# Kernel optimization log

Hardware: AMD Instinct MI355X
Metric: run time of the kernel (lower is better)

## Reference

```python
import jax, jax.numpy as jnp
import numpy as np

B, S, D, H, DFF = 4, 2048, 1024, 8, 4096
DH = D // H  # 128
EPS = 1e-5


def layernorm(x, gamma, beta):
    mu = jnp.mean(x, axis=-1, keepdims=True)
    var = jnp.mean(jnp.square(x - mu), axis=-1, keepdims=True)
    return (x - mu) * jax.lax.rsqrt(var + EPS) * gamma + beta


def setup_inputs() -> dict:
    key = jax.random.key(0)
    ks = jax.random.split(key, 6)
    s = 0.02
    return {
        "src": jax.random.normal(ks[0], (B, S, D), jnp.float32),
        "w_qkv": jax.random.normal(ks[1], (D, 3 * D), jnp.float32) * s,
        "w_out": jax.random.normal(ks[2], (D, D), jnp.float32) * s,
        "w1": jax.random.normal(ks[3], (D, DFF), jnp.float32) * s,
        "b1": jnp.zeros((DFF,), jnp.float32),
        "w2": jax.random.normal(ks[4], (DFF, D), jnp.float32) * s,
        "b2": jnp.zeros((D,), jnp.float32),
        "g1": jnp.ones((D,), jnp.float32),
        "beta1": jnp.zeros((D,), jnp.float32),
        "g2": jnp.ones((D,), jnp.float32),
        "beta2": jnp.zeros((D,), jnp.float32),
    }


def reference(src, w_qkv, w_out, w1, b1, w2, b2, g1, beta1, g2, beta2):
    b, s, d = src.shape
    # --- RingAttention == exact causal MHA on a single device ---
    qkv = src @ w_qkv  # [b, s, 3d]
    q, k, v = jnp.split(qkv, 3, axis=-1)
    to_heads = lambda x: x.reshape(b, s, H, DH).transpose(0, 2, 1, 3)  # [b,h,s,dh]
    q, k, v = to_heads(q), to_heads(k), to_heads(v)
    scale = 1.0 / jnp.sqrt(jnp.asarray(DH, src.dtype))
    scores = jnp.einsum('bhqd,bhkd->bhqk', q, k) * scale  # [b,h,s,s]
    causal = jnp.tril(jnp.ones((s, s), bool))
    neg = jnp.asarray(jnp.finfo(src.dtype).min, src.dtype)
    scores = jnp.where(causal, scores, neg)
    attn = jax.nn.softmax(scores, axis=-1)
    o = jnp.einsum('bhqk,bhkd->bhqd', attn, v)  # [b,h,s,dh]
    o = o.transpose(0, 2, 1, 3).reshape(b, s, d) @ w_out
    # dropout layers are identity at inference
    x = layernorm(src + o, g1, beta1)
    ff = jax.nn.relu(x @ w1 + b1) @ w2 + b2
    return layernorm(x + ff, g2, beta2)
```

## Files before the change

### kernel.cpp

```cpp
#include <hip/hip_runtime.h>

typedef unsigned short u16;
typedef __attribute__((ext_vector_type(8))) short short8;
typedef __attribute__((ext_vector_type(4))) float float4v;

#define MFMA_BF16(a, b, c) __builtin_amdgcn_mfma_f32_16x16x32_bf16((a), (b), (c), 0, 0, 0)

#define B_ 4
#define S_ 2048
#define D_ 1024
#define H_ 8
#define DH_ 128
#define DFF_ 4096
#define EPS_ 1e-5f
#define ROWS_ (B_ * S_)
#define CSCALE_ 0.12751672939502f

__device__ __forceinline__ u16 f2bf(float f) {
  union { float f; unsigned u; } x; x.f = f;
  unsigned r = x.u + 0x7fffu + ((x.u >> 16) & 1u);
  return (u16)(r >> 16);
}

typedef __attribute__((address_space(1))) const unsigned int guint;
typedef __attribute__((address_space(3))) unsigned int luint;
__device__ __forceinline__ void gl2lds16(const u16* g, u16* l) {
  __builtin_amdgcn_global_load_lds((guint*)g, (luint*)l, 16, 0, 0);
}

__global__ void cast_bf16_kernel(const float* __restrict__ in, u16* __restrict__ out, int n4) {
  int i = blockIdx.x * blockDim.x + threadIdx.x;
  int stride = gridDim.x * blockDim.x;
  for (; i < n4; i += stride) {
    float4 v = ((const float4*)in)[i];
    ushort4 u;
    u.x = f2bf(v.x); u.y = f2bf(v.y); u.z = f2bf(v.z); u.w = f2bf(v.w);
    ((ushort4*)out)[i] = u;
  }
}

__global__ void transpose_cast_kernel(const float* __restrict__ in, u16* __restrict__ out,
                                      int K, int N) {
  __shared__ float t[32][33];
  int k0 = blockIdx.x * 32, n0 = blockIdx.y * 32;
  int tx = threadIdx.x & 31, ty = threadIdx.x >> 5;
  #pragma unroll
  for (int i = 0; i < 4; ++i)
    t[ty + 8 * i][tx] = in[(size_t)(k0 + ty + 8 * i) * N + n0 + tx];
  __syncthreads();
  #pragma unroll
  for (int i = 0; i < 4; ++i)
    out[(size_t)(n0 + ty + 8 * i) * K + k0 + tx] = f2bf(t[tx][ty + 8 * i]);
}

__global__ void transpose_v_kernel(const u16* __restrict__ in, u16* __restrict__ out) {
  __shared__ u16 t[32][33];
  int s0 = blockIdx.x * 32, d0 = blockIdx.y * 32, bh = blockIdx.z;
  const u16* src = in + (size_t)bh * S_ * DH_;
  u16* dst = out + (size_t)bh * DH_ * S_;
  int tx = threadIdx.x & 31, ty = threadIdx.x >> 5;
  #pragma unroll
  for (int i = 0; i < 4; ++i)
    t[ty + 8 * i][tx] = src[(size_t)(s0 + ty + 8 * i) * DH_ + d0 + tx];
  __syncthreads();
  #pragma unroll
  for (int i = 0; i < 4; ++i)
    dst[(size_t)(d0 + ty + 8 * i) * S_ + s0 + tx] = t[tx][ty + 8 * i];
}

template <int MODE>
__global__ __launch_bounds__(256) void gemm_kernel(
    const u16* __restrict__ A, const u16* __restrict__ Bt,
    const int M, const int N, const int K,
    float* __restrict__ outF, u16* __restrict__ outH, const float* __restrict__ bias,
    u16* __restrict__ qo, u16* __restrict__ ko, u16* __restrict__ vo) {
  __shared__ u16 As[128][32];
  __shared__ u16 Bs[128][32];
  const int tid = threadIdx.x;
  const int lane = tid & 63, wave = tid >> 6;
  const int quad = lane >> 4, r16 = lane & 15;
  const int wm = (wave >> 1) * 64, wn = (wave & 1) * 64;
  const int m0 = blockIdx.x * 128, n0 = blockIdx.y * 128;

  float4v acc[4][4];
  #pragma unroll
  for (int i = 0; i < 4; ++i)
    #pragma unroll
    for (int j = 0; j < 4; ++j) acc[i][j] = (float4v)0.0f;

  const int srow = lane >> 2, sseg = lane & 3;
  const u16* Ag0 = A + (size_t)(m0 + wave * 32 + srow) * K + sseg * 8;
  const u16* Ag1 = Ag0 + (size_t)16 * K;
  const u16* Bg0 = Bt + (size_t)(n0 + wave * 32 + srow) * K + sseg * 8;
  const u16* Bg1 = Bg0 + (size_t)16 * K;
  u16* Al0 = &As[wave * 32][0];
  u16* Al1 = &As[wave * 32 + 16][0];
  u16* Bl0 = &Bs[wave * 32][0];
  u16* Bl1 = &Bs[wave * 32 + 16][0];

  for (int k0 = 0; k0 < K; k0 += 32) {
    __syncthreads();
    gl2lds16(Ag0 + k0, Al0);
    gl2lds16(Ag1 + k0, Al1);
    gl2lds16(Bg0 + k0, Bl0);
    gl2lds16(Bg1 + k0, Bl1);
    __syncthreads();
    short8 af[4], bf[4];
    #pragma unroll
    for (int t = 0; t < 4; ++t) af[t] = *(const short8*)&As[wm + t * 16 + r16][quad * 8];
    #pragma unroll
    for (int t = 0; t < 4; ++t) bf[t] = *(const short8*)&Bs[wn + t * 16 + r16][quad * 8];
    #pragma unroll
    for (int i = 0; i < 4; ++i)
      #pragma unroll
      for (int j = 0; j < 4; ++j) acc[i][j] = MFMA_BF16(af[i], bf[j], acc[i][j]);
  }

  #pragma unroll
  for (int i = 0; i < 4; ++i) {
    const int rowb = m0 + wm + i * 16 + quad * 4;
    #pragma unroll
    for (int j = 0; j < 4; ++j) {
      const int col = n0 + wn + j * 16 + r16;
      #pragma unroll
      for (int rg = 0; rg < 4; ++rg) {
        float val = acc[i][j][rg];
        const int r = rowb + rg;
        if (MODE == 0) {
          const int part = col >> 10, cc = col & 1023;
          const int h = cc >> 7, dh = cc & 127;
          const int b = r >> 11, s = r & 2047;
          u16* dst = (part == 0) ? qo : (part == 1) ? ko : vo;
          if (part == 0) val *= CSCALE_;
          dst[((size_t)(b * H_ + h) * S_ + s) * DH_ + dh] = f2bf(val);
        } else if (MODE == 1) {
          outF[(size_t)r * N + col] = val;
        } else if (MODE == 2) {
          val += bias[col];
          val = fmaxf(val, 0.0f);
          outH[(size_t)r * N + col] = f2bf(val);
        } else {
          val += bias[col];
          outF[(size_t)r * N + col] = val;
        }
      }
    }
  }
}

__global__ __launch_bounds__(256) void attn_kernel(
    const u16* __restrict__ Q, const u16* __restrict__ Kg,
    const u16* __restrict__ Vtg, u16* __restrict__ O) {
  __shared__ u16 Ks[64][136];
  __shared__ u16 Vt[128][72];
  __shared__ u16 Pw[4][16][72];
  const int tid = threadIdx.x;
  const int lane = tid & 63, wave = tid >> 6;
  const int quad = lane >> 4, r16 = lane & 15;
  const int pairIdx = blockIdx.x;
  const int bh = blockIdx.y;
  const size_t base = (size_t)bh * S_ * DH_;
  const size_t vtb = (size_t)bh * DH_ * S_;
  const int b = bh >> 3, h = bh & 7;

  const u16* kg0 = Kg + base + (size_t)(tid >> 4) * DH_ + (tid & 15) * 8;
  u16* ksl = &Ks[tid >> 4][(tid & 15) * 8];
  const u16* vg0 = Vtg + vtb + (size_t)(tid >> 3) * S_ + (tid & 7) * 8;
  u16* vtl = &Vt[tid >> 3][(tid & 7) * 8];

  for (int half = 0; half < 2; ++half) {
    const int qb = (half == 0) ? pairIdx : 31 - pairIdx;
    const int qr = qb * 64 + wave * 16 + r16;

    short8 aq[4];
    #pragma unroll
    for (int ks = 0; ks < 4; ++ks)
      aq[ks] = *(const short8*)(Q + base + (size_t)qr * DH_ + ks * 32 + quad * 8);

    float4v acco[8];
    #pragma unroll
    for (int i = 0; i < 8; ++i) acco[i] = (float4v)0.0f;
    float m_q = -1e30f, l_q = 0.0f;

    for (int kb = 0; kb <= qb; ++kb) {
      __syncthreads();
      #pragma unroll
      for (int i = 0; i < 4; ++i)
        *(short8*)(ksl + i * 16 * 136) =
            *(const short8*)(kg0 + (size_t)(kb * 64 + i * 16) * DH_);
      #pragma unroll
      for (int i = 0; i < 4; ++i)
        *(short8*)(vtl + i * 32 * 72) =
            *(const short8*)(vg0 + (size_t)i * 32 * S_ + kb * 64);
      __syncthreads();

      float4v accs[4];
      #pragma unroll
      for (int t = 0; t < 4; ++t) accs[t] = (float4v)0.0f;
      #pragma unroll
      for (int ks = 0; ks < 4; ++ks) {
        #pragma unroll
        for (int t = 0; t < 4; ++t) {
          short8 ak = *(const short8*)&Ks[t * 16 + r16][ks * 32 + quad * 8];
          accs[t] = MFMA_BF16(ak, aq[ks], accs[t]);
        }
      }
      if (kb == qb) {
        #pragma unroll
        for (int t = 0; t < 4; ++t)
          #pragma unroll
          for (int rg = 0; rg < 4; ++rg) {
            int kc = kb * 64 + t * 16 + quad * 4 + rg;
            if (kc > qr) accs[t][rg] = -1e30f;
          }
      }
      float mv = accs[0][0];
      #pragma unroll
      for (int t = 0; t < 4; ++t)
        #pragma unroll
        for (int rg = 0; rg < 4; ++rg) mv = fmaxf(mv, accs[t][rg]);
      mv = fmaxf(mv, __shfl_xor(mv, 16));
      mv = fmaxf(mv, __shfl_xor(mv, 32));
      const float mnew = fmaxf(m_q, mv);
      const float alpha = __builtin_amdgcn_exp2f(m_q - mnew);
      float s0 = 0.0f;
      #pragma unroll
      for (int t = 0; t < 4; ++t)
        #pragma unroll
        for (int rg = 0; rg < 4; ++rg) {
          float p = __builtin_amdgcn_exp2f(accs[t][rg] - mnew);
          accs[t][rg] = p;
          s0 += p;
        }
      s0 += __shfl_xor(s0, 16);
      s0 += __shfl_xor(s0, 32);
      l_q = l_q * alpha + s0;
      m_q = mnew;

      #pragma unroll
      for (int t = 0; t < 4; ++t) {
        union { float f; unsigned u; } c0, c1, c2, c3;
        c0.f = accs[t][0]; c1.f = accs[t][1]; c2.f = accs[t][2]; c3.f = accs[t][3];
        uint2 pk;
        pk.x = ((c0.u + 0x8000u) >> 16) | ((c1.u + 0x8000u) & 0xffff0000u);
        pk.y = ((c2.u + 0x8000u) >> 16) | ((c3.u + 0x8000u) & 0xffff0000u);
        *(uint2*)&Pw[wave][r16][t * 16 + quad * 4] = pk;
      }
      float al[4];
      #pragma unroll
      for (int rg = 0; rg < 4; ++rg) al[rg] = __shfl(alpha, quad * 4 + rg);
      #pragma unroll
      for (int nt = 0; nt < 8; ++nt)
        #pragma unroll
        for (int rg = 0; rg < 4; ++rg) acco[nt][rg] *= al[rg];
      asm volatile("s_waitcnt lgkmcnt(0)" ::: "memory");
      #pragma unroll
      for (int ks2 = 0; ks2 < 2; ++ks2) {
        short8 ap = *(const short8*)&Pw[wave][r16][ks2 * 32 + quad * 8];
        #pragma unroll
        for (int nt = 0; nt < 8; ++nt) {
          short8 bv = *(const short8*)&Vt[nt * 16 + r16][ks2 * 32 + quad * 8];
          acco[nt] = MFMA_BF16(ap, bv, acco[nt]);
        }
      }
    }

    float lr[4];
    #pragma unroll
    for (int rg = 0; rg < 4; ++rg) lr[rg] = __shfl(l_q, quad * 4 + rg);
    const int sbase = qb * 64 + wave * 16 + quad * 4;
    #pragma unroll
    for (int nt = 0; nt < 8; ++nt)
      #pragma unroll
      for (int rg = 0; rg < 4; ++rg) {
        float val = acco[nt][rg] / lr[rg];
        O[((size_t)(b * S_ + sbase + rg)) * D_ + h * DH_ + nt * 16 + r16] = f2bf(val);
      }
  }
}

__global__ __launch_bounds__(256) void ln_kernel(
    const float* __restrict__ a, const float* __restrict__ res,
    const float* __restrict__ g, const float* __restrict__ be,
    float* __restrict__ xf, u16* __restrict__ xb) {
  __shared__ float red[8];
  const int row = blockIdx.x, tid = threadIdx.x;
  const float4 va = ((const float4*)(a + (size_t)row * D_))[tid];
  const float4 vr = ((const float4*)(res + (size_t)row * D_))[tid];
  float4 v;
  v.x = va.x + vr.x; v.y = va.y + vr.y; v.z = va.z + vr.z; v.w = va.w + vr.w;
  float s = v.x + v.y + v.z + v.w;
  float q = v.x * v.x + v.y * v.y + v.z * v.z + v.w * v.w;
  #pragma unroll
  for (int m = 1; m < 64; m <<= 1) {
    s += __shfl_xor(s, m);
    q += __shfl_xor(q, m);
  }
  const int wave = tid >> 6, lane = tid & 63;
  if (lane == 0) { red[wave] = s; red[4 + wave] = q; }
  __syncthreads();
  s = red[0] + red[1] + red[2] + red[3];
  q = red[4] + red[5] + red[6] + red[7];
  const float mu = s * (1.0f / D_);
  const float var = q * (1.0f / D_) - mu * mu;
  const float inv = rsqrtf(var + EPS_);
  const float4 gg = ((const float4*)g)[tid];
  const float4 bb = ((const float4*)be)[tid];
  float4 y;
  y.x = (v.x - mu) * inv * gg.x + bb.x;
  y.y = (v.y - mu) * inv * gg.y + bb.y;
  y.z = (v.z - mu) * inv * gg.z + bb.z;
  y.w = (v.w - mu) * inv * gg.w + bb.w;
  ((float4*)(xf + (size_t)row * D_))[tid] = y;
  if (xb) {
    ushort4 u;
    u.x = f2bf(y.x); u.y = f2bf(y.y); u.z = f2bf(y.z); u.w = f2bf(y.w);
    ((ushort4*)(xb + (size_t)row * D_))[tid] = u;
  }
}

extern "C" void kernel_launch(void* const* d_in, const int* in_sizes, int n_in,
                              void* d_out, int out_size, void* d_ws, size_t ws_size,
                              hipStream_t stream) {
  const float* src   = (const float*)d_in[0];
  const float* w_qkv = (const float*)d_in[1];
  const float* w_out = (const float*)d_in[2];
  const float* w1    = (const float*)d_in[3];
  const float* b1    = (const float*)d_in[4];
  const float* w2    = (const float*)d_in[5];
  const float* b2    = (const float*)d_in[6];
  const float* g1    = (const float*)d_in[7];
  const float* be1   = (const float*)d_in[8];
  const float* g2    = (const float*)d_in[9];
  const float* be2   = (const float*)d_in[10];
  float* out = (float*)d_out;

  char* ws = (char*)d_ws;
  size_t off = 0;
  auto alloc = [&](size_t bytes) -> void* {
    void* p = ws + off;
    off += (bytes + 255) & ~(size_t)255;
    return p;
  };
  u16* src_bf = (u16*)alloc((size_t)ROWS_ * D_ * 2);
  u16* wqkvT  = (u16*)alloc((size_t)3 * D_ * D_ * 2);
  u16* woutT  = (u16*)alloc((size_t)D_ * D_ * 2);
  u16* w1T    = (u16*)alloc((size_t)DFF_ * D_ * 2);
  u16* w2T    = (u16*)alloc((size_t)D_ * DFF_ * 2);
  u16* qbuf   = (u16*)alloc((size_t)ROWS_ * D_ * 2);
  u16* kbuf   = (u16*)alloc((size_t)ROWS_ * D_ * 2);
  u16* vbuf   = (u16*)alloc((size_t)ROWS_ * D_ * 2);
  u16* obuf   = (u16*)alloc((size_t)ROWS_ * D_ * 2);
  u16* vT     = (u16*)alloc((size_t)ROWS_ * D_ * 2);
  float* proj = (float*)alloc((size_t)ROWS_ * D_ * 4);
  float* xf   = (float*)alloc((size_t)ROWS_ * D_ * 4);
  u16* xb     = (u16*)alloc((size_t)ROWS_ * D_ * 2);
  u16* h1     = qbuf;
  float* ff   = proj;

  cast_bf16_kernel<<<2048, 256, 0, stream>>>(src, src_bf, ROWS_ * D_ / 4);
  transpose_cast_kernel<<<dim3(D_ / 32, 3 * D_ / 32), 256, 0, stream>>>(w_qkv, wqkvT, D_, 3 * D_);
  transpose_cast_kernel<<<dim3(D_ / 32, D_ / 32), 256, 0, stream>>>(w_out, woutT, D_, D_);
  transpose_cast_kernel<<<dim3(D_ / 32, DFF_ / 32), 256, 0, stream>>>(w1, w1T, D_, DFF_);
  transpose_cast_kernel<<<dim3(DFF_ / 32, D_ / 32), 256, 0, stream>>>(w2, w2T, DFF_, D_);

  gemm_kernel<0><<<dim3(ROWS_ / 128, 3 * D_ / 128), 256, 0, stream>>>(
      src_bf, wqkvT, ROWS_, 3 * D_, D_, nullptr, nullptr, nullptr, qbuf, kbuf, vbuf);
  transpose_v_kernel<<<dim3(S_ / 32, DH_ / 32, B_ * H_), 256, 0, stream>>>(vbuf, vT);
  attn_kernel<<<dim3(16, B_ * H_), 256, 0, stream>>>(qbuf, kbuf, vT, obuf);
  gemm_kernel<1><<<dim3(ROWS_ / 128, D_ / 128), 256, 0, stream>>>(
      obuf, woutT, ROWS_, D_, D_, proj, nullptr, nullptr, nullptr, nullptr, nullptr);
  ln_kernel<<<ROWS_, 256, 0, stream>>>(proj, src, g1, be1, xf, xb);
  gemm_kernel<2><<<dim3(ROWS_ / 128, DFF_ / 128), 256, 0, stream>>>(
      xb, w1T, ROWS_, DFF_, D_, nullptr, h1, b1, nullptr, nullptr, nullptr);
  gemm_kernel<3><<<dim3(ROWS_ / 128, D_ / 128), 256, 0, stream>>>(
      h1, w2T, ROWS_, D_, DFF_, ff, nullptr, b2, nullptr, nullptr, nullptr);
  ln_kernel<<<ROWS_, 256, 0, stream>>>(ff, xf, g2, be2, out, nullptr);
}
```

Baseline: 550.0 us.

## Double-buffer B tiles, load A fragments from global, fuse residual into GEMM epilogue

The GEMM now keeps only the B tile in a double-buffered LDS array and prefetches the next tile while computing the current one, which removes one of the two barriers per K step. A fragments are loaded directly from global memory into registers and prefetched one step ahead. The residual add moves from the layernorm kernel into the out-projection and FFN2 GEMM epilogues, and K becomes a template parameter so loops can unroll. In exchange, A is now read with per-lane strided global loads (each 16-row fragment hits many cache lines), with no LDS sharing across the waves that use the same rows, and register pressure goes up.

```diff
diff --git a/kernel.cpp b/kernel.cpp
--- a/kernel.cpp
+++ b/kernel.cpp
@@ -68,19 +68,20 @@
     dst[(size_t)(d0 + ty + 8 * i) * S_ + s0 + tx] = t[tx][ty + 8 * i];
 }
 
-template <int MODE>
+template <int MODE, int KT>
 __global__ __launch_bounds__(256) void gemm_kernel(
     const u16* __restrict__ A, const u16* __restrict__ Bt,
-    const int M, const int N, const int K,
+    const int M, const int N,
     float* __restrict__ outF, u16* __restrict__ outH, const float* __restrict__ bias,
+    const float* __restrict__ resid,
     u16* __restrict__ qo, u16* __restrict__ ko, u16* __restrict__ vo) {
-  __shared__ u16 As[128][32];
-  __shared__ u16 Bs[128][32];
+  __shared__ u16 Bs[2][128][32];
   const int tid = threadIdx.x;
   const int lane = tid & 63, wave = tid >> 6;
   const int quad = lane >> 4, r16 = lane & 15;
   const int wm = (wave >> 1) * 64, wn = (wave & 1) * 64;
   const int m0 = blockIdx.x * 128, n0 = blockIdx.y * 128;
+  const int K = KT, niter = KT >> 5;
 
   float4v acc[4][4];
   #pragma unroll
@@ -89,31 +90,44 @@
     for (int j = 0; j < 4; ++j) acc[i][j] = (float4v)0.0f;
 
   const int srow = lane >> 2, sseg = lane & 3;
-  const u16* Ag0 = A + (size_t)(m0 + wave * 32 + srow) * K + sseg * 8;
-  const u16* Ag1 = Ag0 + (size_t)16 * K;
   const u16* Bg0 = Bt + (size_t)(n0 + wave * 32 + srow) * K + sseg * 8;
   const u16* Bg1 = Bg0 + (size_t)16 * K;
-  u16* Al0 = &As[wave * 32][0];
-  u16* Al1 = &As[wave * 32 + 16][0];
-  u16* Bl0 = &Bs[wave * 32][0];
-  u16* Bl1 = &Bs[wave * 32 + 16][0];
-
-  for (int k0 = 0; k0 < K; k0 += 32) {
+  u16* Bl0 = &Bs[0][wave * 32][0];
+  u16* Bl1 = &Bs[0][wave * 32 + 16][0];
+  const size_t bufStep = (size_t)128 * 32;
+
+  const u16* Ap[4];
+  #pragma unroll
+  for (int t = 0; t < 4; ++t)
+    Ap[t] = A + (size_t)(m0 + wm + t * 16 + r16) * K + quad * 8;
+
+  gl2lds16(Bg0, Bl0);
+  gl2lds16(Bg1, Bl1);
+  short8 a_cur[4], a_next[4];
+  #pragma unroll
+  for (int t = 0; t < 4; ++t) a_cur[t] = *(const short8*)(Ap[t]);
+
+  #pragma unroll 4
+  for (int i = 0; i < niter; ++i) {
     __syncthreads();
-    gl2lds16(Ag0 + k0, Al0);
-    gl2lds16(Ag1 + k0, Al1);
-    gl2lds16(Bg0 + k0, Bl0);
-    gl2lds16(Bg1 + k0, Bl1);
-    __syncthreads();
-    short8 af[4], bf[4];
-    #pragma unroll
-    for (int t = 0; t < 4; ++t) af[t] = *(const short8*)&As[wm + t * 16 + r16][quad * 8];
-    #pragma unroll
-    for (int t = 0; t < 4; ++t) bf[t] = *(const short8*)&Bs[wn + t * 16 + r16][quad * 8];
-    #pragma unroll
-    for (int i = 0; i < 4; ++i)
-      #pragma unroll
-      for (int j = 0; j < 4; ++j) acc[i][j] = MFMA_BF16(af[i], bf[j], acc[i][j]);
+    if (i + 1 < niter) {
+      const int k1 = (i + 1) << 5;
+      const size_t bo = ((i + 1) & 1) ? bufStep : 0;
+      gl2lds16(Bg0 + k1, Bl0 + bo);
+      gl2lds16(Bg1 + k1, Bl1 + bo);
+      #pragma unroll
+      for (int t = 0; t < 4; ++t) a_next[t] = *(const short8*)(Ap[t] + k1);
+    }
+    short8 bf[4];
+    #pragma unroll
+    for (int t = 0; t < 4; ++t)
+      bf[t] = *(const short8*)&Bs[i & 1][wn + t * 16 + r16][quad * 8];
+    #pragma unroll
+    for (int ii = 0; ii < 4; ++ii)
+      #pragma unroll
+      for (int j = 0; j < 4; ++j) acc[ii][j] = MFMA_BF16(a_cur[ii], bf[j], acc[ii][j]);
+    #pragma unroll
+    for (int t = 0; t < 4; ++t) a_cur[t] = a_next[t];
   }
 
   #pragma unroll
@@ -134,13 +148,14 @@
           if (part == 0) val *= CSCALE_;
           dst[((size_t)(b * H_ + h) * S_ + s) * DH_ + dh] = f2bf(val);
         } else if (MODE == 1) {
+          val += resid[(size_t)r * N + col];
           outF[(size_t)r * N + col] = val;
         } else if (MODE == 2) {
           val += bias[col];
           val = fmaxf(val, 0.0f);
           outH[(size_t)r * N + col] = f2bf(val);
         } else {
-          val += bias[col];
+          val += bias[col] + resid[(size_t)r * N + col];
           outF[(size_t)r * N + col] = val;
         }
       }
@@ -285,10 +300,11 @@
     float* __restrict__ xf, u16* __restrict__ xb) {
   __shared__ float red[8];
   const int row = blockIdx.x, tid = threadIdx.x;
-  const float4 va = ((const float4*)(a + (size_t)row * D_))[tid];
-  const float4 vr = ((const float4*)(res + (size_t)row * D_))[tid];
-  float4 v;
-  v.x = va.x + vr.x; v.y = va.y + vr.y; v.z = va.z + vr.z; v.w = va.w + vr.w;
+  float4 v = ((const float4*)(a + (size_t)row * D_))[tid];
+  if (res) {
+    const float4 vr = ((const float4*)(res + (size_t)row * D_))[tid];
+    v.x += vr.x; v.y += vr.y; v.z += vr.z; v.w += vr.w;
+  }
   float s = v.x + v.y + v.z + v.w;
   float q = v.x * v.x + v.y * v.y + v.z * v.z + v.w * v.w;
   #pragma unroll
@@ -364,16 +380,16 @@
   transpose_cast_kernel<<<dim3(D_ / 32, DFF_ / 32), 256, 0, stream>>>(w1, w1T, D_, DFF_);
   transpose_cast_kernel<<<dim3(DFF_ / 32, D_ / 32), 256, 0, stream>>>(w2, w2T, DFF_, D_);
 
-  gemm_kernel<0><<<dim3(ROWS_ / 128, 3 * D_ / 128), 256, 0, stream>>>(
-      src_bf, wqkvT, ROWS_, 3 * D_, D_, nullptr, nullptr, nullptr, qbuf, kbuf, vbuf);
+  gemm_kernel<0, 1024><<<dim3(ROWS_ / 128, 3 * D_ / 128), 256, 0, stream>>>(
+      src_bf, wqkvT, ROWS_, 3 * D_, nullptr, nullptr, nullptr, nullptr, qbuf, kbuf, vbuf);
   transpose_v_kernel<<<dim3(S_ / 32, DH_ / 32, B_ * H_), 256, 0, stream>>>(vbuf, vT);
   attn_kernel<<<dim3(16, B_ * H_), 256, 0, stream>>>(qbuf, kbuf, vT, obuf);
-  gemm_kernel<1><<<dim3(ROWS_ / 128, D_ / 128), 256, 0, stream>>>(
-      obuf, woutT, ROWS_, D_, D_, proj, nullptr, nullptr, nullptr, nullptr, nullptr);
-  ln_kernel<<<ROWS_, 256, 0, stream>>>(proj, src, g1, be1, xf, xb);
-  gemm_kernel<2><<<dim3(ROWS_ / 128, DFF_ / 128), 256, 0, stream>>>(
-      xb, w1T, ROWS_, DFF_, D_, nullptr, h1, b1, nullptr, nullptr, nullptr);
-  gemm_kernel<3><<<dim3(ROWS_ / 128, D_ / 128), 256, 0, stream>>>(
-      h1, w2T, ROWS_, D_, DFF_, ff, nullptr, b2, nullptr, nullptr, nullptr);
-  ln_kernel<<<ROWS_, 256, 0, stream>>>(ff, xf, g2, be2, out, nullptr);
-}
+  gemm_kernel<1, 1024><<<dim3(ROWS_ / 128, D_ / 128), 256, 0, stream>>>(
+      obuf, woutT, ROWS_, D_, proj, nullptr, nullptr, src, nullptr, nullptr, nullptr);
+  ln_kernel<<<ROWS_, 256, 0, stream>>>(proj, nullptr, g1, be1, xf, xb);
+  gemm_kernel<2, 1024><<<dim3(ROWS_ / 128, DFF_ / 128), 256, 0, stream>>>(
+      xb, w1T, ROWS_, DFF_, nullptr, h1, b1, nullptr, nullptr, nullptr, nullptr);
+  gemm_kernel<3, 4096><<<dim3(ROWS_ / 128, D_ / 128), 256, 0, stream>>>(
+      h1, w2T, ROWS_, D_, ff, nullptr, b2, xf, nullptr, nullptr, nullptr);
+  ln_kernel<<<ROWS_, 256, 0, stream>>>(ff, nullptr, g2, be2, out, nullptr);
+}
```

After: 712.4 us. 1.3x slower.
